# Kernel optimization log

Measured on AMD Instinct MI355X. Metric: run time of the kernel, lower is better.

The kernel has to match this reference:

```python
import jax, jax.numpy as jnp
import numpy as np

VOCAB = 400000
DIM = 300
NUM_QUERIES = 512
TOP_K = 5


def setup_inputs() -> dict:
    key = jax.random.key(0)
    k1, k2 = jax.random.split(key)
    embedding = jax.random.normal(k1, (VOCAB, DIM), dtype=jnp.float32)
    word_ids = jax.random.randint(k2, (NUM_QUERIES,), 0, VOCAB, dtype=jnp.int64)
    return {"embedding": embedding, "word_ids": word_ids, "k": TOP_K}


def reference(embedding, word_ids, k):
    # Row-normalize the table (done in Synonym.__init__: emb / emb.norm(dim=1, keepdim=True))
    E = embedding / jnp.linalg.norm(embedding, axis=1, keepdims=True)  # [V, d]
    # Per-word GEMV against the full table, batched over queries:
    # torch.mm(word_embedding.view(1,-1), embedding.t()) per word -> [Q, V]
    q = E[word_ids]                      # [Q, d] gather of query word vectors
    sims = jnp.einsum('qd,vd->qv', q, E)  # [Q, V] cosine similarities
    # topk(k, largest=True); the torch code sorts results by value afterwards,
    # lax.top_k already returns values in descending order.
    top_vals, top_ids = jax.lax.top_k(sims, k)  # [Q, k], [Q, k]
    return top_vals, top_ids
```

## Files before the change

### kernel.cpp

```cpp
#include <hip/hip_runtime.h>


#define VOCAB   400000
#define DIM     300
#define NQ      512
#define NT      25000
#define TILE_U  5120
#define QFSTR   304
#define TOPK    5
#define NCAND   3072

using f32x4 = __attribute__((ext_vector_type(4))) float;
using s16x8 = __attribute__((ext_vector_type(8))) short;

__device__ __forceinline__ unsigned short f2bf(float f) {
  unsigned int u = __builtin_bit_cast(unsigned int, f);
  u += 0x7fffu + ((u >> 16) & 1u);
  return (unsigned short)(u >> 16);
}

__device__ __forceinline__ void ins3(float v, int id, float* tv, int* ti) {
  if (v > tv[2]) {
    if (v > tv[0]) {
      tv[2] = tv[1]; ti[2] = ti[1]; tv[1] = tv[0]; ti[1] = ti[0];
      tv[0] = v; ti[0] = id;
    } else if (v > tv[1]) {
      tv[2] = tv[1]; ti[2] = ti[1]; tv[1] = v; ti[1] = id;
    } else {
      tv[2] = v; ti[2] = id;
    }
  }
}

__global__ __launch_bounds__(64)
void qprep_kernel(const float* __restrict__ emb, const int* __restrict__ wid,
                  float* __restrict__ qf, unsigned short* __restrict__ qsw) {
  const int q = blockIdx.x;
  const int lane = threadIdx.x;
  const long long w = (long long)wid[q];
  const float* row = emb + w * DIM;
  float x[5];
  double ss = 0.0;
#pragma unroll
  for (int j = 0; j < 5; ++j) {
    const int k = lane + 64 * j;
    x[j] = (k < DIM) ? row[k] : 0.0f;
    ss += (double)x[j] * (double)x[j];
  }
#pragma unroll
  for (int m = 1; m < 64; m <<= 1) ss += __shfl_xor(ss, m, 64);
  const double rinv = 1.0 / sqrt(ss);
#pragma unroll
  for (int j = 0; j < 5; ++j) {
    const int k = lane + 64 * j;
    if (k < DIM) qf[q * QFSTR + k] = (float)((double)x[j] * rinv);
  }
  if (lane < 40) {
    const int ks = lane >> 2, grp = lane & 3;
    const int k0 = ks * 32 + grp * 8;
    unsigned int pw[4];
#pragma unroll
    for (int h = 0; h < 4; ++h) {
      const int k = k0 + 2 * h;
      float v0 = 0.f, v1 = 0.f;
      if (k < DIM)     v0 = (float)((double)row[k] * rinv);
      if (k + 1 < DIM) v1 = (float)((double)row[k + 1] * rinv);
      pw[h] = (unsigned int)f2bf(v0) | ((unsigned int)f2bf(v1) << 16);
    }
    uint4 pk; pk.x = pw[0]; pk.y = pw[1]; pk.z = pw[2]; pk.w = pw[3];
    *(uint4*)(qsw + (size_t)(q >> 4) * TILE_U + ks * 512 + grp * 128 + (q & 15) * 8) = pk;
  }
}

__global__ __launch_bounds__(256)
void prenorm_kernel(const float* __restrict__ emb, unsigned short* __restrict__ sw) {
  __shared__ __align__(16) float rows[64 * 300];

  const int tid = threadIdx.x;
  const int bid = blockIdx.x;
  {
    const f32x4* src = (const f32x4*)(emb + (size_t)bid * 64 * 300);
    f32x4* dst = (f32x4*)rows;
#pragma unroll
    for (int i = 0; i < 19; ++i) {
      const int idx = tid + 256 * i;
      if (idx < 4800) dst[idx] = src[idx];
    }
  }
  __syncthreads();

  const int wave = tid >> 6, lane = tid & 63;
  const int t = bid * 4 + wave;
  const int r = lane & 15, grp = lane >> 4;
  const float* row = rows + (wave * 16 + r) * 300;

  float x[10][8];
  float ss = 0.f;
#pragma unroll
  for (int ks = 0; ks < 10; ++ks) {
    const int k0 = ks * 32 + grp * 8;
    if (k0 + 8 <= DIM) {
      const f32x4 u = *(const f32x4*)(row + k0);
      const f32x4 v = *(const f32x4*)(row + k0 + 4);
#pragma unroll
      for (int j = 0; j < 4; ++j) { x[ks][j] = u[j]; x[ks][j + 4] = v[j]; }
    } else {
#pragma unroll
      for (int j = 0; j < 8; ++j) {
        const int k = k0 + j;
        x[ks][j] = (k < DIM) ? row[k] : 0.0f;
      }
    }
#pragma unroll
    for (int j = 0; j < 8; ++j) ss += x[ks][j] * x[ks][j];
  }
  ss += __shfl_xor(ss, 16, 64);
  ss += __shfl_xor(ss, 32, 64);
  const float rinv = rsqrtf(ss);

  unsigned short* dst = sw + (size_t)t * TILE_U + lane * 8;
#pragma unroll
  for (int ks = 0; ks < 10; ++ks) {
    uint4 pk;
    unsigned int w0 = f2bf(x[ks][0] * rinv) | ((unsigned int)f2bf(x[ks][1] * rinv) << 16);
    unsigned int w1 = f2bf(x[ks][2] * rinv) | ((unsigned int)f2bf(x[ks][3] * rinv) << 16);
    unsigned int w2 = f2bf(x[ks][4] * rinv) | ((unsigned int)f2bf(x[ks][5] * rinv) << 16);
    unsigned int w3 = f2bf(x[ks][6] * rinv) | ((unsigned int)f2bf(x[ks][7] * rinv) << 16);
    pk.x = w0; pk.y = w1; pk.z = w2; pk.w = w3;
    *(uint4*)(dst + ks * 512) = pk;
  }
}

__global__ __launch_bounds__(512, 4)
void score_kernel(const unsigned short* __restrict__ sw,
                  const unsigned short* __restrict__ qsw,
                  float2* __restrict__ cand) {
  __shared__ __align__(16) unsigned short qlds[8 * TILE_U];

  const int tid = threadIdx.x;
  const int wave = tid >> 6, lane = tid & 63;
  const int l15 = lane & 15, grp = lane >> 4;
  const int bid = blockIdx.x;
  const int rest = bid >> 3;
  const int m = rest & 3;
  const int s = (bid & 7) | ((rest >> 2) << 3);
  const int wr = wave >> 1, qhalf = wave & 1;

  {
    const uint4* src = (const uint4*)(qsw + (size_t)m * 8 * TILE_U);
    uint4* dst = (uint4*)qlds;
#pragma unroll
    for (int i = 0; i < 10; ++i) dst[tid + 512 * i] = src[tid + 512 * i];
  }
  __syncthreads();

  float v3[4][3]; int i3[4][3];
#pragma unroll
  for (int qi = 0; qi < 4; ++qi)
#pragma unroll
    for (int j = 0; j < 3; ++j) { v3[qi][j] = -1e30f; i3[qi][j] = 0; }

  const unsigned short* aw = sw + lane * 8;
  const unsigned short* bw = qlds + (size_t)qhalf * 4 * TILE_U + lane * 8;
  const int wt = s * 8 + wr * 2;
  const int nit = (s < 53) ? 25 : 24;

  s16x8 ab[2][2];
  {
    const unsigned w0 = (unsigned)wt * TILE_U;
    ab[0][0] = *(const s16x8*)(aw + w0);
    ab[0][1] = *(const s16x8*)(aw + w0 + TILE_U);
    ab[1][0] = *(const s16x8*)(aw + w0 + 512);
    ab[1][1] = *(const s16x8*)(aw + w0 + TILE_U + 512);
  }

  for (int it = 0; it < nit; ++it) {
    const int t0 = it * 1024 + wt;
    const unsigned toff = (unsigned)t0 * TILE_U;

    f32x4 acc[4][2];
#pragma unroll
    for (int qi = 0; qi < 4; ++qi) {
      acc[qi][0] = {0.f, 0.f, 0.f, 0.f};
      acc[qi][1] = {0.f, 0.f, 0.f, 0.f};
    }

#pragma unroll
    for (int ks = 0; ks < 10; ++ks) {
      unsigned poff;
      if (ks < 8) {
        poff = toff + (unsigned)(ks + 2) * 512;
      } else {
        const unsigned ntoff =
            (it + 1 < nit) ? toff + 1024u * TILE_U : (unsigned)wt * TILE_U;
        poff = ntoff + (unsigned)(ks - 8) * 512;
      }
      const s16x8 p0 = *(const s16x8*)(aw + poff);
      const s16x8 p1 = *(const s16x8*)(aw + poff + TILE_U);

      const unsigned short* bb = bw + ks * 512;
#pragma unroll
      for (int qi = 0; qi < 4; ++qi) {
        const s16x8 b = *(const s16x8*)(bb + qi * TILE_U);
        acc[qi][0] = __builtin_amdgcn_mfma_f32_16x16x32_bf16(ab[ks & 1][0], b, acc[qi][0], 0, 0, 0);
        acc[qi][1] = __builtin_amdgcn_mfma_f32_16x16x32_bf16(ab[ks & 1][1], b, acc[qi][1], 0, 0, 0);
      }
      ab[ks & 1][0] = p0;
      ab[ks & 1][1] = p1;
    }

#pragma unroll
    for (int vi = 0; vi < 2; ++vi) {
      const int rbase = (t0 + vi) * 16 + grp * 4;
#pragma unroll
      for (int qi = 0; qi < 4; ++qi) {
        const f32x4 a4 = acc[qi][vi];
        const float m01 = fmaxf(a4[0], a4[1]);
        const float m23 = fmaxf(a4[2], a4[3]);
        if (fmaxf(m01, m23) > v3[qi][2]) {
#pragma unroll
          for (int rr = 0; rr < 4; ++rr)
            ins3(a4[rr], rbase + rr, &v3[qi][0], &i3[qi][0]);
        }
      }
    }
  }

#pragma unroll
  for (int qi = 0; qi < 4; ++qi) {
    float m0 = v3[qi][0], m1 = v3[qi][1], m2 = v3[qi][2];
    int   d0 = i3[qi][0], d1 = i3[qi][1], d2 = i3[qi][2];
    const int q = m * 128 + qhalf * 64 + qi * 16 + l15;
    float2* dst = cand + (size_t)q * NCAND + ((s * 4 + wr) * 6);
#pragma unroll
    for (int r = 0; r < 6; ++r) {
      float bv = m0; int bi = d0; int bl = grp;
      float ov = __shfl_xor(bv, 16, 64);
      int   oi = __shfl_xor(bi, 16, 64);
      int   ol = __shfl_xor(bl, 16, 64);
      if (ov > bv || (ov == bv && ol < bl)) { bv = ov; bi = oi; bl = ol; }
      ov = __shfl_xor(bv, 32, 64);
      oi = __shfl_xor(bi, 32, 64);
      ol = __shfl_xor(bl, 32, 64);
      if (ov > bv || (ov == bv && ol < bl)) { bv = ov; bi = oi; bl = ol; }
      if (bl == grp) { m0 = m1; d0 = d1; m1 = m2; d1 = d2; m2 = -1e30f; }
      if (r == grp || r == grp + 4) {
        float2 e; e.x = bv; e.y = __int_as_float(bi);
        dst[r] = e;
      }
    }
  }
}

__global__ __launch_bounds__(256)
void topk_kernel(const float* __restrict__ emb, const float* __restrict__ qf,
                 const float2* __restrict__ cand, float* __restrict__ out) {
  __shared__ float pV[256 * 6];
  __shared__ int   pI[256 * 6];
  __shared__ int   selI[32];
  __shared__ float resV[32];

  const int q = blockIdx.x;
  const int t = threadIdx.x;
  const float2* cq = cand + (size_t)q * NCAND;

  float bv[6]; int bi[6];
#pragma unroll
  for (int j = 0; j < 6; ++j) { bv[j] = -1e30f; bi[j] = -1; }
  for (int i = t; i < NCAND; i += 256) {
    const float2 e = cq[i];
    const float v = e.x;
    if (v > bv[5]) {
      bv[5] = v; bi[5] = __float_as_int(e.y);
#pragma unroll
      for (int j = 5; j > 0; --j) {
        if (bv[j] > bv[j - 1]) {
          const float tv2 = bv[j]; bv[j] = bv[j - 1]; bv[j - 1] = tv2;
          const int ti2 = bi[j]; bi[j] = bi[j - 1]; bi[j - 1] = ti2;
        }
      }
    }
  }
#pragma unroll
  for (int j = 0; j < 6; ++j) { pV[t * 6 + j] = bv[j]; pI[t * 6 + j] = bi[j]; }
  __syncthreads();

  if (t < 64) {
    for (int r = 0; r < 32; ++r) {
      float mv = -2e30f; int mp = 0;
      for (int i = t; i < 256 * 6; i += 64) {
        const float v = pV[i];
        if (v > mv) { mv = v; mp = i; }
      }
#pragma unroll
      for (int m = 1; m < 64; m <<= 1) {
        const float ov = __shfl_xor(mv, m, 64);
        const int   op = __shfl_xor(mp, m, 64);
        if (ov > mv) { mv = ov; mp = op; }
      }
      if (t == 0) { selI[r] = pI[mp]; pV[mp] = -2e30f; }
      __builtin_amdgcn_wave_barrier();
    }
  }
  __syncthreads();

  {
    const int j = t >> 3, sub = t & 7;
    const int id = selI[j];
    float dot = 0.f, sq = 0.f;
    if (id >= 0) {
      const f32x4* e4 = (const f32x4*)(emb + (size_t)id * DIM);
      const f32x4* q4 = (const f32x4*)(qf + (size_t)q * QFSTR);
      for (int f = sub; f < DIM / 4; f += 8) {
        const f32x4 ev = e4[f], qv = q4[f];
        dot += ev[0]*qv[0] + ev[1]*qv[1] + ev[2]*qv[2] + ev[3]*qv[3];
        sq  += ev[0]*ev[0] + ev[1]*ev[1] + ev[2]*ev[2] + ev[3]*ev[3];
      }
    }
#pragma unroll
    for (int m = 1; m < 8; m <<= 1) {
      dot += __shfl_xor(dot, m, 64);
      sq  += __shfl_xor(sq, m, 64);
    }
    if (sub == 0)
      resV[j] = (id >= 0 && sq > 0.f) ? (float)((double)dot / sqrt((double)sq)) : -2e30f;
  }
  __syncthreads();

  if (t == 0) {
#pragma unroll
    for (int r = 0; r < TOPK; ++r) {
      float mv = -3e30f; int mp = 0;
      for (int i = 0; i < 32; ++i) if (resV[i] > mv) { mv = resV[i]; mp = i; }
      out[q * TOPK + r] = mv;
      out[NQ * TOPK + q * TOPK + r] = (float)selI[mp];
      resV[mp] = -3e30f;
    }
  }
}

extern "C" void kernel_launch(void* const* d_in, const int* in_sizes, int n_in,
                              void* d_out, int out_size, void* d_ws, size_t ws_size,
                              hipStream_t stream) {
  (void)in_sizes; (void)n_in; (void)out_size; (void)ws_size;
  const float* emb = (const float*)d_in[0];
  const int* wid = (const int*)d_in[1];
  float* out = (float*)d_out;

  char* ws = (char*)d_ws;
  unsigned short* qsw = (unsigned short*)ws;
  float*  qf   = (float*)(ws + 327680);
  float2* cand = (float2*)(ws + 950272);
  unsigned short* sw = (unsigned short*)(ws + 13533184);

  qprep_kernel<<<NQ, 64, 0, stream>>>(emb, wid, qf, qsw);
  prenorm_kernel<<<VOCAB / 64, 256, 0, stream>>>(emb, sw);
  score_kernel<<<512, 512, 0, stream>>>(sw, qsw, cand);
  topk_kernel<<<NQ, 256, 0, stream>>>(emb, qf, cand, out);
}
```

Measured before the change: 1.293 ms.

## Double-buffer whole tile-pair banks in registers and halve occupancy bound

Replaces the rolling two-slice prefetch with full-tile register double-buffering: while one tile pair's 20 A fragments are consumed by MFMAs, the next pair's fragments are loaded into a second bank. Launch bounds drop from 4 to 2 blocks per CU so the roughly 80 extra VGPRs fit. The aim is deeper memory-level parallelism to hide global load latency on the table stream. The cost is lower occupancy, so fewer waves are available to hide latency. The nit condition is rewritten as wt<424, which equals the previous s<53 test.

```diff
diff --git a/kernel.cpp b/kernel.cpp
--- a/kernel.cpp
+++ b/kernel.cpp
@@ -131,7 +131,55 @@
   }
 }
 
-__global__ __launch_bounds__(512, 4)
+
+__device__ __forceinline__ void load_bank(s16x8 (&bank)[2][10],
+                                          const unsigned short* __restrict__ aw,
+                                          unsigned toff) {
+#pragma unroll
+  for (int ks = 0; ks < 10; ++ks) {
+    bank[0][ks] = *(const s16x8*)(aw + toff + ks * 512);
+    bank[1][ks] = *(const s16x8*)(aw + toff + TILE_U + ks * 512);
+  }
+}
+
+__device__ __forceinline__ void compute_pair(const s16x8 (&bank)[2][10],
+                                             const unsigned short* __restrict__ bw,
+                                             int t0, int grp,
+                                             float (&v3)[4][3], int (&i3)[4][3]) {
+  f32x4 acc[4][2];
+#pragma unroll
+  for (int qi = 0; qi < 4; ++qi) {
+    acc[qi][0] = {0.f, 0.f, 0.f, 0.f};
+    acc[qi][1] = {0.f, 0.f, 0.f, 0.f};
+  }
+#pragma unroll
+  for (int ks = 0; ks < 10; ++ks) {
+    const unsigned short* bb = bw + ks * 512;
+#pragma unroll
+    for (int qi = 0; qi < 4; ++qi) {
+      const s16x8 b = *(const s16x8*)(bb + qi * TILE_U);
+      acc[qi][0] = __builtin_amdgcn_mfma_f32_16x16x32_bf16(bank[0][ks], b, acc[qi][0], 0, 0, 0);
+      acc[qi][1] = __builtin_amdgcn_mfma_f32_16x16x32_bf16(bank[1][ks], b, acc[qi][1], 0, 0, 0);
+    }
+  }
+#pragma unroll
+  for (int vi = 0; vi < 2; ++vi) {
+    const int rbase = (t0 + vi) * 16 + grp * 4;
+#pragma unroll
+    for (int qi = 0; qi < 4; ++qi) {
+      const f32x4 a4 = acc[qi][vi];
+      const float m01 = fmaxf(a4[0], a4[1]);
+      const float m23 = fmaxf(a4[2], a4[3]);
+      if (fmaxf(m01, m23) > v3[qi][2]) {
+#pragma unroll
+        for (int rr = 0; rr < 4; ++rr)
+          ins3(a4[rr], rbase + rr, &v3[qi][0], &i3[qi][0]);
+      }
+    }
+  }
+}
+
+__global__ __launch_bounds__(512, 2)
 void score_kernel(const unsigned short* __restrict__ sw,
                   const unsigned short* __restrict__ qsw,
                   float2* __restrict__ cand) {
@@ -163,68 +211,24 @@
   const unsigned short* aw = sw + lane * 8;
   const unsigned short* bw = qlds + (size_t)qhalf * 4 * TILE_U + lane * 8;
   const int wt = s * 8 + wr * 2;
-  const int nit = (s < 53) ? 25 : 24;
-
-  s16x8 ab[2][2];
-  {
-    const unsigned w0 = (unsigned)wt * TILE_U;
-    ab[0][0] = *(const s16x8*)(aw + w0);
-    ab[0][1] = *(const s16x8*)(aw + w0 + TILE_U);
-    ab[1][0] = *(const s16x8*)(aw + w0 + 512);
-    ab[1][1] = *(const s16x8*)(aw + w0 + TILE_U + 512);
-  }
-
-  for (int it = 0; it < nit; ++it) {
-    const int t0 = it * 1024 + wt;
-    const unsigned toff = (unsigned)t0 * TILE_U;
-
-    f32x4 acc[4][2];
-#pragma unroll
-    for (int qi = 0; qi < 4; ++qi) {
-      acc[qi][0] = {0.f, 0.f, 0.f, 0.f};
-      acc[qi][1] = {0.f, 0.f, 0.f, 0.f};
-    }
-
-#pragma unroll
-    for (int ks = 0; ks < 10; ++ks) {
-      unsigned poff;
-      if (ks < 8) {
-        poff = toff + (unsigned)(ks + 2) * 512;
-      } else {
-        const unsigned ntoff =
-            (it + 1 < nit) ? toff + 1024u * TILE_U : (unsigned)wt * TILE_U;
-        poff = ntoff + (unsigned)(ks - 8) * 512;
-      }
-      const s16x8 p0 = *(const s16x8*)(aw + poff);
-      const s16x8 p1 = *(const s16x8*)(aw + poff + TILE_U);
-
-      const unsigned short* bb = bw + ks * 512;
-#pragma unroll
-      for (int qi = 0; qi < 4; ++qi) {
-        const s16x8 b = *(const s16x8*)(bb + qi * TILE_U);
-        acc[qi][0] = __builtin_amdgcn_mfma_f32_16x16x32_bf16(ab[ks & 1][0], b, acc[qi][0], 0, 0, 0);
-        acc[qi][1] = __builtin_amdgcn_mfma_f32_16x16x32_bf16(ab[ks & 1][1], b, acc[qi][1], 0, 0, 0);
-      }
-      ab[ks & 1][0] = p0;
-      ab[ks & 1][1] = p1;
-    }
-
-#pragma unroll
-    for (int vi = 0; vi < 2; ++vi) {
-      const int rbase = (t0 + vi) * 16 + grp * 4;
-#pragma unroll
-      for (int qi = 0; qi < 4; ++qi) {
-        const f32x4 a4 = acc[qi][vi];
-        const float m01 = fmaxf(a4[0], a4[1]);
-        const float m23 = fmaxf(a4[2], a4[3]);
-        if (fmaxf(m01, m23) > v3[qi][2]) {
-#pragma unroll
-          for (int rr = 0; rr < 4; ++rr)
-            ins3(a4[rr], rbase + rr, &v3[qi][0], &i3[qi][0]);
-        }
-      }
-    }
-  }
+  const int nit = (wt < 424) ? 25 : 24;
+
+  s16x8 A0[2][10], A1[2][10];
+  load_bank(A0, aw, (unsigned)wt * TILE_U);
+
+  int it = 0;
+  while (it + 1 < nit) {
+    load_bank(A1, aw, (unsigned)((it + 1) * 1024 + wt) * TILE_U);
+    compute_pair(A0, bw, it * 1024 + wt, grp, v3, i3);
+    {
+      const int nt2 = (it + 2 < nit) ? (it + 2) * 1024 + wt : wt;
+      load_bank(A0, aw, (unsigned)nt2 * TILE_U);
+    }
+    compute_pair(A1, bw, (it + 1) * 1024 + wt, grp, v3, i3);
+    it += 2;
+  }
+  if (it < nit)
+    compute_pair(A0, bw, it * 1024 + wt, grp, v3, i3);
 
 #pragma unroll
   for (int qi = 0; qi < 4; ++qi) {
```

Result: faster. 1.093 ms (-15.5%).
